# Kernel tuning notes

Hardware: AMD Instinct MI355X
Metric: run time of the kernel (lower is better)

## Reference

```python
import jax, jax.numpy as jnp
import numpy as np

B, S, D = 8, 2048, 512  # batch, seq_len, input_dim == qk_dim
K_SIZE = 6


def setup_inputs() -> dict:
    key = jax.random.key(0)
    ks = jax.random.split(key, 8)
    return {
        "evo_local": jax.random.normal(ks[0], (B, S, D), dtype=jnp.float32),
        "Wq": jax.random.normal(ks[1], (D, D), dtype=jnp.float32) * (1.0 / np.sqrt(D)),
        "bq": jax.random.normal(ks[2], (D,), dtype=jnp.float32) * 0.02,
        "dw_w": jax.random.normal(ks[3], (D, 1, K_SIZE), dtype=jnp.float32) * 0.1,  # depthwise conv (O, I/groups=1, K)
        "dw_b": jax.random.normal(ks[4], (D,), dtype=jnp.float32) * 0.02,
        "pw_w": jax.random.normal(ks[5], (D, D), dtype=jnp.float32) * (1.0 / np.sqrt(D)),  # pointwise 1x1 conv as matrix
        "pw_b": jax.random.normal(ks[6], (D,), dtype=jnp.float32) * 0.02,
        "pos": jax.random.normal(ks[7], (1, S, D), dtype=jnp.float32),
    }


def reference(evo_local, Wq, bq, dw_w, dw_b, pw_w, pw_b, pos):
    d = evo_local.shape[-1]
    # Q = Linear(evo_local) + learned positional encoding
    Q = jnp.einsum("bsd,ed->bse", evo_local, Wq) + bq + pos  # [B,S,D]

    # depthwise conv1d, kernel=6, torch padding='same' for even kernel -> pad (2, 3)
    x = jnp.transpose(evo_local, (0, 2, 1))  # [B,D,S]
    kv = jax.lax.conv_general_dilated(
        x, dw_w,
        window_strides=(1,),
        padding=[(2, 3)],
        feature_group_count=d,
        dimension_numbers=("NCH", "OIH", "NCH"),
    ) + dw_b[None, :, None]  # [B,D,S]
    # pointwise 1x1 conv
    kv = jnp.einsum("od,bds->bos", pw_w, kv) + pw_b[None, :, None]  # [B,D,S]
    KV = jnp.transpose(kv, (0, 2, 1))  # [B,S,D]; K and V share this

    scale = 1.0 / jnp.sqrt(jnp.float32(d))
    scores = jnp.einsum("bsd,btd->bst", Q, KV) * scale  # [B,S,S]
    attn = jax.nn.softmax(scores, axis=-1)
    out = jnp.einsum("bst,btd->bsd", attn, KV)
    return out + KV + evo_local
```

## Files before the change

### kernel.cpp

```cpp
#include <hip/hip_runtime.h>


typedef unsigned short ushort_t;
typedef __attribute__((ext_vector_type(8))) short short8;
typedef __attribute__((ext_vector_type(8))) unsigned short u16x8;
typedef __attribute__((ext_vector_type(4))) float f32x4;
typedef float4 f4;

__device__ __forceinline__ float bf2f(ushort_t h) {
    union { unsigned u; float f; } v; v.u = ((unsigned)h) << 16; return v.f;
}
__device__ __forceinline__ ushort_t f2bf(float f) {
    union { float f; unsigned u; } v; v.f = f;
    unsigned r = (v.u + 0x7FFFu + ((v.u >> 16) & 1u)) >> 16;
    return (ushort_t)r;
}

__device__ __forceinline__ void gld_lds16(const void* g, void* l) {
    __builtin_amdgcn_global_load_lds((const __attribute__((address_space(1))) void*)g,
                                     (__attribute__((address_space(3))) void*)l, 16, 0, 0);
}

#define BAR()   asm volatile("s_barrier" ::: "memory")
#define WAITV8  do { asm volatile("s_waitcnt vmcnt(8)" ::: "memory"); __builtin_amdgcn_sched_barrier(0); } while (0)
#define WAITV0  do { asm volatile("s_waitcnt vmcnt(0)" ::: "memory"); __builtin_amdgcn_sched_barrier(0); } while (0)
#define WAITL   do { asm volatile("s_waitcnt lgkmcnt(0)" ::: "memory"); __builtin_amdgcn_sched_barrier(0); } while (0)

template<int EPI>
__global__ __launch_bounds__(512, 2)
void mfma_nt256(const ushort_t* __restrict__ A, long long sA, int ldA,
                const ushort_t* __restrict__ B, long long sB, int ldB,
                int N, int K, float alpha,
                ushort_t* __restrict__ Ch, long long sC,
                float* __restrict__ Cf,
                const ushort_t* __restrict__ addH,
                const float* __restrict__ addF, long long sAdd)
{
    __shared__ __align__(16) ushort_t lds[65536];

    const int t = threadIdx.x;
    const int w = t >> 6, lane = t & 63;

    int tx, ty, z;
    if (EPI == 2) {
        const int lin = blockIdx.x + (blockIdx.y << 3) + (blockIdx.z << 6);
        const int xcd = lin & 7;
        const int s   = lin >> 3;
        z  = s >> 3;
        const int j = s & 7;
        ty = 2 * (xcd & 3) + (j >> 2);
        tx = 4 * (xcd >> 2) + (j & 3);
    } else {
        const int lin = blockIdx.x + (blockIdx.y << 1) + (blockIdx.z << 4);
        ty = lin & 7;
        tx = (lin >> 3) & 1;
        z  = lin >> 4;
    }
    A += (long long)z * sA;
    B += (long long)z * sB;
    const int m0 = ty * 256, n0 = tx * 256;

    const int wr = w >> 2, wc = w & 3;
    const int fr = lane & 15, kg = lane >> 4;
    const int nkt = K >> 6;

    const int sRo = lane >> 2;
    const long long sCk = ((lane & 3) ^ ((lane >> 3) & 3)) * 8;
    const int co = (kg ^ ((fr >> 1) & 3)) * 8;

#define STAGE(P, base0, ld, segbase, h, Ts) do {                                         \
    const long long kk_ = (long long)(((Ts) < nkt ? (Ts) : (nkt - 1)) * 64 + (h) * 32) + sCk; \
    const int g0_ = w * 2;                                                               \
    gld_lds16((P) + (long long)((base0) + g0_ * 16 + sRo) * (ld) + kk_,                  \
              &lds[(segbase) + g0_ * 512]);                                              \
    gld_lds16((P) + (long long)((base0) + g0_ * 16 + 16 + sRo) * (ld) + kk_,             \
              &lds[(segbase) + g0_ * 512 + 512]);                                        \
} while (0)

#define AREAD(ksseg) do {                                                                \
    const int ab_ = (ksseg) * 8192 + wr * 4096 + fr * 32 + co;                           \
    _Pragma("unroll") for (int fm_ = 0; fm_ < 8; ++fm_)                                  \
        afr[fm_] = *(const short8*)&lds[ab_ + fm_ * 512];                                \
} while (0)

#define BREAD(ksseg, fnh) do {                                                           \
    const int bb_ = 32768 + (ksseg) * 8192 + wc * 2048 + (fnh) * 1024 + fr * 32 + co;    \
    bfr[0] = *(const short8*)&lds[bb_];                                                  \
    bfr[1] = *(const short8*)&lds[bb_ + 512];                                            \
} while (0)

#define MF2(j0) do {                                                                     \
    __builtin_amdgcn_s_setprio(1);                                                       \
    _Pragma("unroll") for (int fm_ = 0; fm_ < 8; ++fm_) {                                \
        acc[fm_][(j0)]     = __builtin_amdgcn_mfma_f32_16x16x32_bf16(afr[fm_], bfr[0], acc[fm_][(j0)], 0, 0, 0);     \
        acc[fm_][(j0) + 1] = __builtin_amdgcn_mfma_f32_16x16x32_bf16(afr[fm_], bfr[1], acc[fm_][(j0) + 1], 0, 0, 0); \
    }                                                                                    \
    __builtin_amdgcn_s_setprio(0);                                                       \
} while (0)

    const f32x4 zero = {0.f, 0.f, 0.f, 0.f};
    f32x4 acc[8][4];
#pragma unroll
    for (int i = 0; i < 8; ++i)
#pragma unroll
        for (int j = 0; j < 4; ++j) acc[i][j] = zero;

    short8 afr[8], bfr[2];

    STAGE(A, m0, ldA, 0,             0, 0);
    STAGE(B, n0, ldB, 32768,         0, 0);
    STAGE(A, m0, ldA, 8192,          1, 0);
    STAGE(B, n0, ldB, 32768 + 8192,  1, 0);
    STAGE(A, m0, ldA, 16384,         0, 1);
    STAGE(B, n0, ldB, 32768 + 16384, 0, 1);
    WAITV8;
    BAR();

    for (int kt = 0; kt < nkt; ++kt) {
        const int b = kt & 1, nb = b ^ 1;
        AREAD(b * 2); BREAD(b * 2, 0);
        STAGE(A, m0, ldA, (nb * 2 + 1) * 8192, 1, kt + 1);
        BAR(); WAITL;
        MF2(0);
        BAR();
        BREAD(b * 2, 1);
        STAGE(B, n0, ldB, 32768 + (nb * 2 + 1) * 8192, 1, kt + 1);
        BAR(); WAITL;
        MF2(2);
        WAITV8;
        BAR();
        AREAD(b * 2 + 1); BREAD(b * 2 + 1, 0);
        STAGE(A, m0, ldA, (b * 2) * 8192, 0, kt + 2);
        BAR(); WAITL;
        MF2(0);
        BAR();
        BREAD(b * 2 + 1, 1);
        STAGE(B, n0, ldB, 32768 + (b * 2) * 8192, 0, kt + 2);
        BAR(); WAITL;
        MF2(2);
        WAITV8;
        BAR();
    }
    WAITV0;

#pragma unroll
    for (int fm = 0; fm < 8; ++fm)
#pragma unroll
    for (int fn = 0; fn < 4; ++fn)
#pragma unroll
    for (int r = 0; r < 4; ++r) {
        const int m = m0 + wr * 128 + fm * 16 + kg * 4 + r;
        const int n = n0 + wc * 64 + fn * 16 + fr;
        float v = acc[fm][fn][r];
        const long long idx = (long long)m * N + n;
        if (EPI == 2) {
            Ch[(long long)z * sC + idx] = f2bf(v * alpha);
        } else {
            const long long o = (long long)z * sAdd + idx;
            v += bf2f(addH[o]) + addF[o];
            Cf[o] = v;
        }
    }
#undef STAGE
#undef AREAD
#undef BREAD
#undef MF2
}

template<int AF32, int EPI>
__global__ __launch_bounds__(256)
void mfma_nt(const void* __restrict__ Aptr, long long sA, int ldA,
             const ushort_t* __restrict__ Bh, long long sB, int ldB,
             int N, int K, float alpha,
             const float* __restrict__ bias, const float* __restrict__ pos,
             ushort_t* __restrict__ Ch, ushort_t* __restrict__ CTh,
             long long sC)
{
    __shared__ __align__(16) ushort_t lds[8192];
    ushort_t* lAh = lds;
    ushort_t* lBh = lds + 4096;

    const int t = threadIdx.x;
    const int w = t >> 6, lane = t & 63;
    const int z = blockIdx.z;
    const ushort_t* Ab = (const ushort_t*)Aptr + (long long)z * sA;
    const float*    Af = (const float*)Aptr    + (long long)z * sA;
    Bh += (long long)z * sB;

    const int m0 = blockIdx.y * 128, n0 = blockIdx.x * 128;
    const int wr = w >> 1, wc = w & 1;
    const int fr = lane & 15, kg = lane >> 4;
    const int srow = lane >> 2;
    const int scol = (lane & 3) * 8;

    const f32x4 zero = {0.f, 0.f, 0.f, 0.f};
    f32x4 acc[4][4];
#pragma unroll
    for (int i = 0; i < 4; ++i)
#pragma unroll
        for (int j = 0; j < 4; ++j) acc[i][j] = zero;

    for (int k0 = 0; k0 < K; k0 += 32) {
#pragma unroll
        for (int i = 0; i < 2; ++i) {
            const int g = w * 2 + i;
            const int row = g * 16 + srow;
            if (AF32) {
                const float* p = Af + (long long)(m0 + row) * ldA + k0 + scol;
                f4 v0 = *(const f4*)p;
                f4 v1 = *(const f4*)(p + 4);
                u16x8 o;
                o[0] = f2bf(v0.x); o[1] = f2bf(v0.y); o[2] = f2bf(v0.z); o[3] = f2bf(v0.w);
                o[4] = f2bf(v1.x); o[5] = f2bf(v1.y); o[6] = f2bf(v1.z); o[7] = f2bf(v1.w);
                *(u16x8*)&lAh[g * 512 + srow * 32 + scol] = o;
            } else {
                gld_lds16(Ab + (long long)(m0 + row) * ldA + k0 + scol, &lAh[g * 512]);
            }
            gld_lds16(Bh + (long long)(n0 + row) * ldB + k0 + scol, &lBh[g * 512]);
        }
        __syncthreads();

        short8 aH[4];
#pragma unroll
        for (int fm = 0; fm < 4; ++fm)
            aH[fm] = *(const short8*)&lAh[(wr * 64 + fm * 16 + fr) * 32 + kg * 8];
#pragma unroll
        for (int fn = 0; fn < 4; ++fn) {
            short8 bH = *(const short8*)&lBh[(wc * 64 + fn * 16 + fr) * 32 + kg * 8];
#pragma unroll
            for (int fm = 0; fm < 4; ++fm)
                acc[fm][fn] = __builtin_amdgcn_mfma_f32_16x16x32_bf16(aH[fm], bH, acc[fm][fn], 0, 0, 0);
        }
        __syncthreads();
    }

#pragma unroll
    for (int fm = 0; fm < 4; ++fm)
#pragma unroll
    for (int fn = 0; fn < 4; ++fn)
#pragma unroll
    for (int r = 0; r < 4; ++r) {
        const int m = m0 + wr * 64 + fm * 16 + kg * 4 + r;
        const int n = n0 + wc * 64 + fn * 16 + fr;
        float v = acc[fm][fn][r];
        const long long idx = (long long)m * N + n;
        if (EPI == 0) {
            v += bias[n] + pos[(long long)(m & 2047) * N + n];
            Ch[idx] = f2bf(v);
        } else {
            v += bias[n];
            ushort_t hi = f2bf(v);
            Ch[idx] = hi;
            CTh[(long long)(m >> 11) * (512LL * 2048) + (long long)n * 2048 + (m & 2047)] = hi;
        }
    }
}

__global__ __launch_bounds__(256)
void cvt2_bf16(const float* __restrict__ a, ushort_t* __restrict__ ao,
               const float* __restrict__ b, ushort_t* __restrict__ bo)
{
    int i = blockIdx.x * 256 + threadIdx.x;
    const float* src = (i < 65536) ? a : b;
    ushort_t* dst = (i < 65536) ? ao : bo;
    int j = i & 65535;
    f4 v = *(const f4*)(src + (long long)j * 4);
    ushort4 o;
    o.x = f2bf(v.x); o.y = f2bf(v.y); o.z = f2bf(v.z); o.w = f2bf(v.w);
    *(ushort4*)&dst[(long long)j * 4] = o;
}

__global__ __launch_bounds__(256)
void dwconv_bf16(const float* __restrict__ x, const float* __restrict__ w,
                 const float* __restrict__ bias, ushort_t* __restrict__ y)
{
    const int tid = blockIdx.x * 256 + threadIdx.x;
    const int d4 = tid & 127;
    const int rest = tid >> 7;
    const int sc = rest & 255;
    const int b = rest >> 8;
    const int s0 = sc * 8;
    const float* xb = x + ((long long)b * 2048) * 512 + d4 * 4;

    f4 win[13];
#pragma unroll
    for (int j = 0; j < 13; ++j) {
        int r = s0 + j - 2;
        int rc = r < 0 ? 0 : (r > 2047 ? 2047 : r);
        f4 v = *(const f4*)(xb + (long long)rc * 512);
        if (r < 0 || r > 2047) { v.x = 0.f; v.y = 0.f; v.z = 0.f; v.w = 0.f; }
        win[j] = v;
    }
    float wk[4][6];
#pragma unroll
    for (int dd = 0; dd < 4; ++dd)
#pragma unroll
        for (int k = 0; k < 6; ++k) wk[dd][k] = w[(d4 * 4 + dd) * 6 + k];
    const f4 bs4 = *(const f4*)(bias + d4 * 4);

    ushort_t* yb = y + ((long long)b * 2048 + s0) * 512 + d4 * 4;
#pragma unroll
    for (int u = 0; u < 8; ++u) {
        float a0 = bs4.x, a1 = bs4.y, a2 = bs4.z, a3 = bs4.w;
#pragma unroll
        for (int k = 0; k < 6; ++k) {
            f4 v = win[u + k];
            a0 = fmaf(v.x, wk[0][k], a0);
            a1 = fmaf(v.y, wk[1][k], a1);
            a2 = fmaf(v.z, wk[2][k], a2);
            a3 = fmaf(v.w, wk[3][k], a3);
        }
        ushort4 o;
        o.x = f2bf(a0); o.y = f2bf(a1); o.z = f2bf(a2); o.w = f2bf(a3);
        *(ushort4*)(yb + (long long)u * 512) = o;
    }
}

__global__ __launch_bounds__(256)
void softmax_bf16(ushort_t* __restrict__ p)
{
    ushort_t* row = p + ((long long)blockIdx.x << 11);
    const int t = threadIdx.x;
    __shared__ float redMax[4];
    __shared__ float redSum[4];

    u16x8 u = *(const u16x8*)(row + t * 8);
    float x[8];
#pragma unroll
    for (int i = 0; i < 8; ++i) x[i] = bf2f(u[i]);

    float m = x[0];
#pragma unroll
    for (int i = 1; i < 8; ++i) m = fmaxf(m, x[i]);
#pragma unroll
    for (int off = 32; off > 0; off >>= 1) m = fmaxf(m, __shfl_xor(m, off));
    if ((t & 63) == 0) redMax[t >> 6] = m;
    __syncthreads();
    m = fmaxf(fmaxf(redMax[0], redMax[1]), fmaxf(redMax[2], redMax[3]));

    float e[8], s = 0.f;
#pragma unroll
    for (int i = 0; i < 8; ++i) { e[i] = __expf(x[i] - m); s += e[i]; }
#pragma unroll
    for (int off = 32; off > 0; off >>= 1) s += __shfl_xor(s, off);
    if ((t & 63) == 0) redSum[t >> 6] = s;
    __syncthreads();
    s = (redSum[0] + redSum[1]) + (redSum[2] + redSum[3]);
    const float inv = 1.0f / s;

#pragma unroll
    for (int i = 0; i < 8; ++i) u[i] = f2bf(e[i] * inv);
    *(u16x8*)(row + t * 8) = u;
}

extern "C" void kernel_launch(void* const* d_in, const int* in_sizes, int n_in,
                              void* d_out, int out_size, void* d_ws, size_t ws_size,
                              hipStream_t stream)
{
    const float* evo  = (const float*)d_in[0];
    const float* Wq   = (const float*)d_in[1];
    const float* bq   = (const float*)d_in[2];
    const float* dw_w = (const float*)d_in[3];
    const float* dw_b = (const float*)d_in[4];
    const float* pw_w = (const float*)d_in[5];
    const float* pw_b = (const float*)d_in[6];
    const float* pos  = (const float*)d_in[7];
    float* out = (float*)d_out;

    const long long BSD = 8LL * 2048 * 512;
    const long long DD  = 512LL * 512;
    const long long SD  = 2048LL * 512;
    const long long SS  = 2048LL * 2048;

    ushort_t* QHi  = (ushort_t*)d_ws;
    ushort_t* KVHi = QHi + BSD;
    ushort_t* KVT  = KVHi + BSD;
    ushort_t* WqB  = KVT + BSD;
    ushort_t* pwB  = WqB + DD;
    ushort_t* X    = pwB + DD;

    long long Xbytes = (long long)ws_size - 51380224LL;
    long long cRaw = Xbytes / (SS * 2);
    int c;
    if (cRaw >= 8) c = 8; else if (cRaw >= 4) c = 4; else if (cRaw >= 2) c = 2; else c = 1;

    ushort_t* dwout = X;

    cvt2_bf16<<<512, 256, 0, stream>>>(Wq, WqB, pw_w, pwB);
    dwconv_bf16<<<1024, 256, 0, stream>>>(evo, dw_w, dw_b, dwout);

    mfma_nt<1, 0><<<dim3(4, 128, 1), 256, 0, stream>>>(
        evo, 0LL, 512, WqB, 0LL, 512, 512, 512, 1.f,
        bq, pos, QHi, nullptr, 0LL);

    mfma_nt<0, 1><<<dim3(4, 128, 1), 256, 0, stream>>>(
        dwout, 0LL, 512, pwB, 0LL, 512, 512, 512, 1.f,
        pw_b, nullptr, KVHi, KVT, 0LL);

    const float scale = 0.04419417382415922f;
    for (int b0 = 0; b0 < 8; b0 += c) {
        const int cc = (8 - b0 < c) ? (8 - b0) : c;
        const long long o = (long long)b0 * SD;
        mfma_nt256<2><<<dim3(8, 8, cc), 512, 0, stream>>>(
            QHi + o, SD, 512, KVHi + o, SD, 512, 2048, 512, scale,
            X, SS, nullptr, nullptr, nullptr, 0LL);
        softmax_bf16<<<cc * 2048, 256, 0, stream>>>(X);
        mfma_nt256<3><<<dim3(2, 8, cc), 512, 0, stream>>>(
            X, SS, 2048, KVT + o, SD, 2048, 512, 2048, 1.f,
            nullptr, 0LL, out + o, KVHi + o, evo + o, SD);
    }
}
```

Before: 284.7 us.

## Add 128-row PV GEMM kernel and wave-per-row softmax

After: 273.1 us. 1.04x faster.

```diff
diff --git a/kernel.cpp b/kernel.cpp
--- a/kernel.cpp
+++ b/kernel.cpp
@@ -23,6 +23,7 @@
 
 #define BAR()   asm volatile("s_barrier" ::: "memory")
 #define WAITV8  do { asm volatile("s_waitcnt vmcnt(8)" ::: "memory"); __builtin_amdgcn_sched_barrier(0); } while (0)
+#define WAITV6  do { asm volatile("s_waitcnt vmcnt(6)" ::: "memory"); __builtin_amdgcn_sched_barrier(0); } while (0)
 #define WAITV0  do { asm volatile("s_waitcnt vmcnt(0)" ::: "memory"); __builtin_amdgcn_sched_barrier(0); } while (0)
 #define WAITL   do { asm volatile("s_waitcnt lgkmcnt(0)" ::: "memory"); __builtin_amdgcn_sched_barrier(0); } while (0)
 
@@ -42,7 +43,7 @@
     const int w = t >> 6, lane = t & 63;
 
     int tx, ty, z;
-    if (EPI == 2) {
+    {
         const int lin = blockIdx.x + (blockIdx.y << 3) + (blockIdx.z << 6);
         const int xcd = lin & 7;
         const int s   = lin >> 3;
@@ -50,11 +51,6 @@
         const int j = s & 7;
         ty = 2 * (xcd & 3) + (j >> 2);
         tx = 4 * (xcd >> 2) + (j & 3);
-    } else {
-        const int lin = blockIdx.x + (blockIdx.y << 1) + (blockIdx.z << 4);
-        ty = lin & 7;
-        tx = (lin >> 3) & 1;
-        z  = lin >> 4;
     }
     A += (long long)z * sA;
     B += (long long)z * sB;
@@ -151,20 +147,144 @@
     for (int r = 0; r < 4; ++r) {
         const int m = m0 + wr * 128 + fm * 16 + kg * 4 + r;
         const int n = n0 + wc * 64 + fn * 16 + fr;
-        float v = acc[fm][fn][r];
         const long long idx = (long long)m * N + n;
-        if (EPI == 2) {
-            Ch[(long long)z * sC + idx] = f2bf(v * alpha);
-        } else {
-            const long long o = (long long)z * sAdd + idx;
-            v += bf2f(addH[o]) + addF[o];
-            Cf[o] = v;
-        }
+        Ch[(long long)z * sC + idx] = f2bf(acc[fm][fn][r] * alpha);
     }
 #undef STAGE
 #undef AREAD
 #undef BREAD
 #undef MF2
+}
+
+__global__ __launch_bounds__(512, 1)
+void mfma_pv128(const ushort_t* __restrict__ A, long long sA, int ldA,
+                const ushort_t* __restrict__ B, long long sB, int ldB,
+                int N, int K,
+                float* __restrict__ Cf,
+                const ushort_t* __restrict__ addH,
+                const float* __restrict__ addF, long long sAdd)
+{
+    __shared__ __align__(16) ushort_t lds[49152];
+
+    const int t = threadIdx.x;
+    const int w = t >> 6, lane = t & 63;
+
+    int tx, ty, z;
+    const int lin = blockIdx.x + (blockIdx.y << 1) + (blockIdx.z << 5);
+    if (gridDim.z == 8) {
+        z = lin & 7;
+        const int j = lin >> 3;
+        ty = j >> 1;
+        tx = j & 1;
+    } else {
+        tx = blockIdx.x; ty = blockIdx.y; z = blockIdx.z;
+    }
+    A += (long long)z * sA;
+    B += (long long)z * sB;
+    const int m0 = ty * 128, n0 = tx * 256;
+
+    const int wr = w >> 2, wc = w & 3;
+    const int fr = lane & 15, kg = lane >> 4;
+    const int nkt = K >> 6;
+
+    const int sRo = lane >> 2;
+    const long long sCk = ((lane & 3) ^ ((lane >> 3) & 3)) * 8;
+    const int co = (kg ^ ((fr >> 1) & 3)) * 8;
+
+#define SA_(seg, h, Ts) do {                                                             \
+    const long long kk_ = (long long)(((Ts) < nkt ? (Ts) : (nkt - 1)) * 64 + (h) * 32) + sCk; \
+    gld_lds16(A + (long long)(m0 + w * 16 + sRo) * ldA + kk_,                            \
+              &lds[(seg) * 4096 + w * 512]);                                             \
+} while (0)
+
+#define SB_(seg, h, Ts) do {                                                             \
+    const long long kk_ = (long long)(((Ts) < nkt ? (Ts) : (nkt - 1)) * 64 + (h) * 32) + sCk; \
+    const int g0_ = w * 2;                                                               \
+    gld_lds16(B + (long long)(n0 + g0_ * 16 + sRo) * ldB + kk_,                          \
+              &lds[16384 + (seg) * 8192 + g0_ * 512]);                                   \
+    gld_lds16(B + (long long)(n0 + g0_ * 16 + 16 + sRo) * ldB + kk_,                     \
+              &lds[16384 + (seg) * 8192 + g0_ * 512 + 512]);                             \
+} while (0)
+
+#define AR_(seg) do {                                                                    \
+    const int ab_ = (seg) * 4096 + wr * 2048 + fr * 32 + co;                             \
+    _Pragma("unroll") for (int fm_ = 0; fm_ < 4; ++fm_)                                  \
+        afr[fm_] = *(const short8*)&lds[ab_ + fm_ * 512];                                \
+} while (0)
+
+#define BR_(seg, fnh) do {                                                               \
+    const int bb_ = 16384 + (seg) * 8192 + wc * 2048 + (fnh) * 1024 + fr * 32 + co;      \
+    bfr[0] = *(const short8*)&lds[bb_];                                                  \
+    bfr[1] = *(const short8*)&lds[bb_ + 512];                                            \
+} while (0)
+
+#define MF8(j0) do {                                                                     \
+    __builtin_amdgcn_s_setprio(1);                                                       \
+    _Pragma("unroll") for (int fm_ = 0; fm_ < 4; ++fm_) {                                \
+        acc[fm_][(j0)]     = __builtin_amdgcn_mfma_f32_16x16x32_bf16(afr[fm_], bfr[0], acc[fm_][(j0)], 0, 0, 0);     \
+        acc[fm_][(j0) + 1] = __builtin_amdgcn_mfma_f32_16x16x32_bf16(afr[fm_], bfr[1], acc[fm_][(j0) + 1], 0, 0, 0); \
+    }                                                                                    \
+    __builtin_amdgcn_s_setprio(0);                                                       \
+} while (0)
+
+    const f32x4 zero = {0.f, 0.f, 0.f, 0.f};
+    f32x4 acc[4][4];
+#pragma unroll
+    for (int i = 0; i < 4; ++i)
+#pragma unroll
+        for (int j = 0; j < 4; ++j) acc[i][j] = zero;
+
+    short8 afr[4], bfr[2];
+
+    SA_(0, 0, 0); SB_(0, 0, 0);
+    SA_(1, 1, 0); SB_(1, 1, 0);
+    SA_(2, 0, 1); SB_(2, 0, 1);
+    WAITV6;
+    BAR();
+
+    for (int kt = 0; kt < nkt; ++kt) {
+        const int b = kt & 1, nb = b ^ 1;
+        AR_(b * 2); BR_(b * 2, 0);
+        SA_(nb * 2 + 1, 1, kt + 1);
+        BAR(); WAITL;
+        MF8(0);
+        BAR();
+        BR_(b * 2, 1);
+        SB_(nb * 2 + 1, 1, kt + 1);
+        BAR(); WAITL;
+        MF8(2);
+        WAITV6;
+        BAR();
+        AR_(b * 2 + 1); BR_(b * 2 + 1, 0);
+        SA_(b * 2, 0, kt + 2);
+        BAR(); WAITL;
+        MF8(0);
+        BAR();
+        BR_(b * 2 + 1, 1);
+        SB_(b * 2, 0, kt + 2);
+        BAR(); WAITL;
+        MF8(2);
+        WAITV6;
+        BAR();
+    }
+    WAITV0;
+
+#pragma unroll
+    for (int fm = 0; fm < 4; ++fm)
+#pragma unroll
+    for (int fn = 0; fn < 4; ++fn)
+#pragma unroll
+    for (int r = 0; r < 4; ++r) {
+        const int m = m0 + wr * 64 + fm * 16 + kg * 4 + r;
+        const int n = n0 + wc * 64 + fn * 16 + fr;
+        const long long o = (long long)z * sAdd + (long long)m * N + n;
+        Cf[o] = acc[fm][fn][r] + bf2f(addH[o]) + addF[o];
+    }
+#undef SA_
+#undef SB_
+#undef AR_
+#undef BR_
+#undef MF8
 }
 
 template<int AF32, int EPI>
@@ -317,40 +437,40 @@
 }
 
 __global__ __launch_bounds__(256)
-void softmax_bf16(ushort_t* __restrict__ p)
-{
-    ushort_t* row = p + ((long long)blockIdx.x << 11);
+void softmax_wave(ushort_t* __restrict__ p)
+{
     const int t = threadIdx.x;
-    __shared__ float redMax[4];
-    __shared__ float redSum[4];
-
-    u16x8 u = *(const u16x8*)(row + t * 8);
-    float x[8];
-#pragma unroll
-    for (int i = 0; i < 8; ++i) x[i] = bf2f(u[i]);
+    const int w = t >> 6, lane = t & 63;
+    ushort_t* row = p + (((long long)blockIdx.x * 4 + w) << 11);
+
+    u16x8 u[4];
+    float x[32];
+#pragma unroll
+    for (int i = 0; i < 4; ++i) {
+        u[i] = *(const u16x8*)(row + i * 512 + lane * 8);
+#pragma unroll
+        for (int j = 0; j < 8; ++j) x[i * 8 + j] = bf2f(u[i][j]);
+    }
 
     float m = x[0];
 #pragma unroll
-    for (int i = 1; i < 8; ++i) m = fmaxf(m, x[i]);
+    for (int i = 1; i < 32; ++i) m = fmaxf(m, x[i]);
 #pragma unroll
     for (int off = 32; off > 0; off >>= 1) m = fmaxf(m, __shfl_xor(m, off));
-    if ((t & 63) == 0) redMax[t >> 6] = m;
-    __syncthreads();
-    m = fmaxf(fmaxf(redMax[0], redMax[1]), fmaxf(redMax[2], redMax[3]));
-
-    float e[8], s = 0.f;
-#pragma unroll
-    for (int i = 0; i < 8; ++i) { e[i] = __expf(x[i] - m); s += e[i]; }
+
+    float s = 0.f;
+#pragma unroll
+    for (int i = 0; i < 32; ++i) { x[i] = __expf(x[i] - m); s += x[i]; }
 #pragma unroll
     for (int off = 32; off > 0; off >>= 1) s += __shfl_xor(s, off);
-    if ((t & 63) == 0) redSum[t >> 6] = s;
-    __syncthreads();
-    s = (redSum[0] + redSum[1]) + (redSum[2] + redSum[3]);
     const float inv = 1.0f / s;
 
 #pragma unroll
-    for (int i = 0; i < 8; ++i) u[i] = f2bf(e[i] * inv);
-    *(u16x8*)(row + t * 8) = u;
+    for (int i = 0; i < 4; ++i) {
+#pragma unroll
+        for (int j = 0; j < 8; ++j) u[i][j] = f2bf(x[i * 8 + j] * inv);
+        *(u16x8*)(row + i * 512 + lane * 8) = u[i];
+    }
 }
 
 extern "C" void kernel_launch(void* const* d_in, const int* in_sizes, int n_in,
@@ -404,9 +524,9 @@
         mfma_nt256<2><<<dim3(8, 8, cc), 512, 0, stream>>>(
             QHi + o, SD, 512, KVHi + o, SD, 512, 2048, 512, scale,
             X, SS, nullptr, nullptr, nullptr, 0LL);
-        softmax_bf16<<<cc * 2048, 256, 0, stream>>>(X);
-        mfma_nt256<3><<<dim3(2, 8, cc), 512, 0, stream>>>(
-            X, SS, 2048, KVT + o, SD, 2048, 512, 2048, 1.f,
-            nullptr, 0LL, out + o, KVHi + o, evo + o, SD);
-    }
-}
+        softmax_wave<<<cc * 512, 256, 0, stream>>>(X);
+        mfma_pv128<<<dim3(2, 16, cc), 512, 0, stream>>>(
+            X, SS, 2048, KVT + o, SD, 2048, 512, 2048,
+            out + o, KVHi + o, evo + o, SD);
+    }
+}
```
